# Kernel tuning notes

Measured on AMD Instinct MI355X. Metric: run time of the kernel, lower is better.

## Reference

```python
import jax, jax.numpy as jnp
import numpy as np

N = 384       # nodes
K = 60        # neighbors per node
SUB = 20      # subsample_k
C_S = 128
C_Z = 128
H = 4
D_HEAD = C_Z // H
NUM_RBF = 64
E = N * K
EPS = 1e-8


def _rbf(D, D_min=0.0, D_max=20.0, D_count=NUM_RBF):
    # radial basis expansion of distances: [..., ] -> [..., D_count]
    mu = jnp.linspace(D_min, D_max, D_count)
    sigma = (D_max - D_min) / D_count
    return jnp.exp(-(((D[..., None] - mu) / sigma) ** 2))


def setup_inputs() -> dict:
    key = jax.random.key(0)
    ks = jax.random.split(key, 16)
    f32 = jnp.float32
    inp = {
        "node_features": jax.random.normal(ks[0], (N, C_S), f32),
        "node_trans": jax.random.normal(ks[1], (N, 3), f32) * 5.0,
        "edge_features": jax.random.normal(ks[2], (E, C_Z), f32),
        "edge_index": jax.random.randint(ks[3], (2, E), 0, N),
        "subsample_idx": jax.random.randint(ks[4], (N, K, SUB), 0, K),
        # dist_bias_gate: Linear(2*c_s -> H)
        "W_gate": jax.random.normal(ks[5], (2 * C_S, H), f32) / np.sqrt(2 * C_S),
        "b_gate": jnp.zeros((H,), f32),
        # dist_bias: Linear(num_rbf -> H)
        "W_db": jax.random.normal(ks[6], (NUM_RBF, H), f32) / np.sqrt(NUM_RBF),
        "b_db": jnp.zeros((H,), f32),
        # lin_qk: Linear(c_z -> 2*c_z)
        "W_qk": jax.random.normal(ks[7], (C_Z, 2 * C_Z), f32) / np.sqrt(C_Z),
        "b_qk": jnp.zeros((2 * C_Z,), f32),
        # lin_v: Linear(c_z -> c_z)
        "W_v": jax.random.normal(ks[8], (C_Z, C_Z), f32) / np.sqrt(C_Z),
        "b_v": jnp.zeros((C_Z,), f32),
        # lin_out: Linear(c_z -> c_z) (init='final' in source; random here for testing)
        "W_out": jax.random.normal(ks[9], (C_Z, C_Z), f32) / np.sqrt(C_Z),
        "b_out": jnp.zeros((C_Z,), f32),
    }
    return inp


def reference(node_features, node_trans, edge_features, edge_index, subsample_idx,
              W_gate, b_gate, W_db, b_db, W_qk, b_qk, W_v, b_v, W_out, b_out):
    n, k, sub = subsample_idx.shape
    # assume_sorted=True path: edges are grouped k-per-destination-node
    dst = edge_index[0].reshape(n, k)                           # [n,k] neighbor ids
    edge1 = jnp.broadcast_to(dst[:, :, None], (n, k, sub))      # [n,k,sub]
    edge2 = jnp.take_along_axis(
        jnp.broadcast_to(dst[:, None, :], (n, k, k)), subsample_idx, axis=-1)  # [n,k,sub]

    f1 = node_features[edge1]                                   # [n,k,sub,c_s]
    f2 = node_features[edge2]
    gate = jax.nn.sigmoid(jnp.concatenate([f1, f2], axis=-1) @ W_gate + b_gate)  # [n,k,sub,H]

    t1 = node_trans[edge1]                                      # [n,k,sub,3]
    t2 = node_trans[edge2]
    dist = jnp.linalg.norm(t1 - t2 + EPS, axis=-1)              # [n,k,sub]
    bias = gate * (_rbf(dist) @ W_db + b_db)                    # [n,k,sub,H]

    edges = edge_features.reshape(n, k, C_Z)
    qk = edges @ W_qk + b_qk
    q, kk = jnp.split(qk, 2, axis=-1)
    q = q.reshape(n, k, H, D_HEAD)
    kk = kk.reshape(n, k, H, D_HEAD)

    batch = jnp.arange(n)[:, None, None]
    k_sub = kk[batch, subsample_idx]                            # [n,k,sub,H,d]
    attn = jnp.einsum('nkhd,nkshd->nksh', q, k_sub) / np.sqrt(C_Z) + bias
    attn = jax.nn.softmax(attn, axis=2)                         # softmax over subsample axis

    v = (edges @ W_v + b_v).reshape(n, k, H, D_HEAD)
    v_sub = v[batch, subsample_idx]                             # [n,k,sub,H,d]
    upd = jnp.einsum('nksh,nkshd->nkhd', attn, v_sub).reshape(n * k, C_Z)
    return upd @ W_out + b_out                                  # [E, c_z]
```

## Files before the change

### kernel.cpp

```cpp
#include <hip/hip_runtime.h>
#include <hip/hip_bf16.h>

typedef unsigned short ushortT;
typedef __attribute__((ext_vector_type(8))) short bf16x8;
typedef __attribute__((ext_vector_type(4))) float f32x4;
typedef __attribute__((ext_vector_type(2))) float f32x2;

#define N_NODES 384
#define KNBR 60
#define SUBK 20
#define NEDGE (N_NODES * KNBR)
#define EPSC 1e-8f
#define INV_SQRT_CZ 0.08838834764831845f
#define MU_STEP (20.0f / 63.0f)
#define INV_MU_STEP (63.0f / 20.0f)
#define INV_SIGMA 3.2f

__device__ __forceinline__ float bflo(unsigned int u) { return __uint_as_float(u << 16); }
__device__ __forceinline__ float bfhi(unsigned int u) { return __uint_as_float(u & 0xffff0000u); }
__device__ __forceinline__ f32x2 bfpair(unsigned int u) {
  f32x2 r;
  r.x = bflo(u);
  r.y = bfhi(u);
  return r;
}
__device__ __forceinline__ ushortT f2bu(float v) {
  union { float f; unsigned int u; } c;
  c.f = v;
  return (ushortT)((c.u + 0x7fffu + ((c.u >> 16) & 1u)) >> 16);
}
__device__ __forceinline__ unsigned int pack2bf(float x, float y) {
  return (unsigned int)f2bu(x) | ((unsigned int)f2bu(y) << 16);
}
__device__ __forceinline__ ushortT f2h(float x) {
  _Float16 h = (_Float16)x;
  return __builtin_bit_cast(ushortT, h);
}
__device__ __forceinline__ float h2f(ushortT u) {
  return (float)__builtin_bit_cast(_Float16, u);
}

__global__ __launch_bounds__(256) void prep_kernel(
    const float* __restrict__ nf, const float* __restrict__ Wg, float* __restrict__ g,
    const float* __restrict__ Wqk, const float* __restrict__ bqk,
    const float* __restrict__ Wv, const float* __restrict__ bv,
    const float* __restrict__ Wout,
    ushortT* __restrict__ Wp1, ushortT* __restrict__ Wp2, float* __restrict__ bc) {
  int b = blockIdx.x, tid = threadIdx.x;
  if (b < 96) {
    int n = b * 4 + (tid >> 6), t = tid & 63;
    float a = nf[n * 128 + t];
    float bb = nf[n * 128 + 64 + t];
    float acc[8];
#pragma unroll
    for (int h = 0; h < 4; ++h) {
      acc[h]     = a * Wg[t * 4 + h]         + bb * Wg[(t + 64) * 4 + h];
      acc[4 + h] = a * Wg[(128 + t) * 4 + h] + bb * Wg[(192 + t) * 4 + h];
    }
#pragma unroll
    for (int i = 0; i < 8; ++i)
#pragma unroll
      for (int off = 32; off >= 1; off >>= 1) acc[i] += __shfl_xor(acc[i], off, 64);
    if (t == 0) {
#pragma unroll
      for (int i = 0; i < 8; ++i) g[n * 8 + i] = acc[i];
    }
  } else {
    int i = (b - 96) * 256 + tid;
    if (i < 49152) {
      int j = i & 7, l = (i >> 3) & 63, t = (i >> 9) & 3;
      int nt = (i >> 11) % 12, ny = (i >> 11) / 12;
      int nn = ny * 192 + nt * 16 + (l & 15);
      int k = t * 32 + (l >> 4) * 8 + j;
      float v = (nn < 256) ? Wqk[k * 256 + nn] : Wv[k * 128 + (nn - 256)];
      if (nn < 128) v *= INV_SQRT_CZ;
      Wp1[i] = f2bu(v);
    } else {
      int i2 = i - 49152;
      int j = i2 & 7, l = (i2 >> 3) & 63, t = (i2 >> 9) & 3, nt = (i2 >> 11);
      int nn = nt * 16 + (l & 15);
      int k = t * 32 + (l >> 4) * 8 + j;
      Wp2[i2] = f2bu(Wout[k * 128 + nn]);
    }
    if (i < 384) {
      float v = (i < 256) ? bqk[i] : bv[i - 256];
      if (i < 128) v *= INV_SQRT_CZ;
      bc[i] = v;
    }
  }
}

__global__ __launch_bounds__(512, 4) void fused_kernel(
    const float* __restrict__ ef, const ushortT* __restrict__ Wp1,
    const ushortT* __restrict__ Wp2, const float* __restrict__ bc,
    const float* __restrict__ bout, const float* __restrict__ g,
    const float* __restrict__ node_trans, const int* __restrict__ edge_index,
    const int* __restrict__ sub_idx, const float* __restrict__ W_db,
    const float* __restrict__ b_db, const float* __restrict__ b_gate,
    float* __restrict__ outp) {
  __shared__ __align__(16) ushortT kvb[KNBR * 256];
  __shared__ __align__(16) ushortT updq[64 * 136];
  __shared__ __align__(16) ushortT biasb[KNBR * SUBK * 4];
  __shared__ ushortT sub_lds[KNBR * SUBK];

  int n = blockIdx.x, tid = threadIdx.x;
  int e0 = n * KNBR;
  int w = tid >> 6, l = tid & 63;
  int lr = l & 15, lc = l >> 4;
  int rowA = (w & 3) * 16 + lr;
  int rowAc = min(rowA, KNBR - 1);
  int Tbase = (tid >> 8) * 12;

  bf16x8 bcur[4], bnxt[4];
#pragma unroll
  for (int t = 0; t < 4; ++t)
    bcur[t] = *(const bf16x8*)(Wp1 + ((Tbase * 4 + t) * 64 + l) * 8);

  bf16x8 afrag[4];
#pragma unroll
  for (int t = 0; t < 4; ++t) {
    const float* ap = ef + (size_t)(e0 + rowAc) * 128 + t * 32 + lc * 8;
    float4 lo = *(const float4*)ap;
    float4 hi = *(const float4*)(ap + 4);
    bf16x8 a;
    a[0] = (short)f2bu(lo.x); a[1] = (short)f2bu(lo.y);
    a[2] = (short)f2bu(lo.z); a[3] = (short)f2bu(lo.w);
    a[4] = (short)f2bu(hi.x); a[5] = (short)f2bu(hi.y);
    a[6] = (short)f2bu(hi.z); a[7] = (short)f2bu(hi.w);
    afrag[t] = a;
  }

#pragma unroll
  for (int Ti = 0; Ti < 12; ++Ti) {
    int T = Tbase + Ti;
    if (Ti < 11) {
#pragma unroll
      for (int t = 0; t < 4; ++t)
        bnxt[t] = *(const bf16x8*)(Wp1 + (((T + 1) * 4 + t) * 64 + l) * 8);
    }
    f32x4 acc = {0.f, 0.f, 0.f, 0.f};
#pragma unroll
    for (int t = 0; t < 4; ++t)
      acc = __builtin_amdgcn_mfma_f32_16x16x32_bf16(bcur[t], afrag[t], acc, 0, 0, 0);
    int col0 = T * 16 + lc * 4;
    float4 bi = *(const float4*)(bc + col0);
    float o0 = acc[0] + bi.x, o1 = acc[1] + bi.y;
    float o2 = acc[2] + bi.z, o3 = acc[3] + bi.w;
    uint2 o;
    o.x = pack2bf(o0, o1);
    o.y = pack2bf(o2, o3);
    if (T < 8) {
      *(uint2*)(updq + rowA * 136 + col0) = o;
    } else if (rowA < KNBR) {
      int colk = col0 - 128;
      int base_b = (colk & 128) << 1;
      int d = colk & 127;
      int inner = ((d >> 3) & 1) * 128 + (((d >> 4) * 16) ^ ((rowA & 7) << 4)) + (d & 7) * 2;
      *(uint2*)((char*)kvb + rowA * 512 + base_b + inner) = o;
    }
#pragma unroll
    for (int t = 0; t < 4; ++t) bcur[t] = bnxt[t];
  }

  float4 bgv = *(const float4*)b_gate;
  float4 bdbv = *(const float4*)b_db;
  for (int p = tid; p < KNBR * SUBK; p += 512) {
    int kl = p / SUBK, s = p - kl * SUBK;
    int j = sub_idx[(size_t)(e0 + kl) * SUBK + s];
    sub_lds[p] = (ushortT)j;
    int dk = edge_index[e0 + kl];
    int dj = edge_index[e0 + j];
    float dx = node_trans[dk * 3 + 0] - node_trans[dj * 3 + 0] + EPSC;
    float dy = node_trans[dk * 3 + 1] - node_trans[dj * 3 + 1] + EPSC;
    float dz = node_trans[dk * 3 + 2] - node_trans[dj * 3 + 2] + EPSC;
    float dist = sqrtf(dx * dx + dy * dy + dz * dz);
    int r0 = (int)(dist * INV_MU_STEP + 0.5f);
    int rlo = max(r0 - 4, 0), rhi = min(r0 + 4, 63);
    float a0 = 0.f, a1 = 0.f, a2 = 0.f, a3 = 0.f;
    for (int r = rlo; r <= rhi; ++r) {
      float t = (dist - r * MU_STEP) * INV_SIGMA;
      float e = __expf(-t * t);
      float4 wv = ((const float4*)W_db)[r];
      a0 += e * wv.x; a1 += e * wv.y; a2 += e * wv.z; a3 += e * wv.w;
    }
    float4 gk = *(const float4*)(g + dk * 8);
    float4 gj = *(const float4*)(g + dj * 8 + 4);
    float g1 = gk.x + gj.x + bgv.x;
    float g2 = gk.y + gj.y + bgv.y;
    float g3 = gk.z + gj.z + bgv.z;
    float g4 = gk.w + gj.w + bgv.w;
    biasb[p * 4 + 0] = f2h((a0 + bdbv.x) / (1.0f + __expf(-g1)));
    biasb[p * 4 + 1] = f2h((a1 + bdbv.y) / (1.0f + __expf(-g2)));
    biasb[p * 4 + 2] = f2h((a2 + bdbv.z) / (1.0f + __expf(-g3)));
    biasb[p * 4 + 3] = f2h((a3 + bdbv.w) / (1.0f + __expf(-g4)));
  }
  __syncthreads();

  int row3 = tid >> 3, h = (tid >> 1) & 3, dh = tid & 1;
  int row3c = min(row3, KNBR - 1);
  int hdo = (h * 2 + dh) * 16;
  const char* kvbase = (const char*)kvb;
  f32x2 qv0, qv1, qv2, qv3, qv4, qv5, qv6, qv7;
  {
    const ushortT* qp = updq + row3 * 136 + h * 32 + dh * 16;
    uint4 u0 = *(const uint4*)qp;
    uint4 u1 = *(const uint4*)(qp + 8);
    qv0 = bfpair(u0.x); qv1 = bfpair(u0.y); qv2 = bfpair(u0.z); qv3 = bfpair(u0.w);
    qv4 = bfpair(u1.x); qv5 = bfpair(u1.y); qv6 = bfpair(u1.z); qv7 = bfpair(u1.w);
  }
  float den = 0.f;
  f32x2 va0 = {0.f, 0.f}, va1 = {0.f, 0.f}, va2 = {0.f, 0.f}, va3 = {0.f, 0.f};
  f32x2 va4 = {0.f, 0.f}, va5 = {0.f, 0.f}, va6 = {0.f, 0.f}, va7 = {0.f, 0.f};
#pragma unroll 4
  for (int s = 0; s < SUBK; ++s) {
    int j = sub_lds[row3c * SUBK + s];
    int off = hdo ^ ((j & 7) << 4);
    const char* kr = kvbase + j * 512;
    uint4 k0 = *(const uint4*)(kr + off);
    uint4 k1 = *(const uint4*)(kr + 128 + off);
    f32x2 dacc = qv0 * bfpair(k0.x);
    dacc += qv1 * bfpair(k0.y);
    dacc += qv2 * bfpair(k0.z);
    dacc += qv3 * bfpair(k0.w);
    dacc += qv4 * bfpair(k1.x);
    dacc += qv5 * bfpair(k1.y);
    dacc += qv6 * bfpair(k1.z);
    dacc += qv7 * bfpair(k1.w);
    float dot = dacc.x + dacc.y;
    dot += __shfl_xor(dot, 1);
    float p = __expf(dot + h2f(biasb[(row3c * SUBK + s) * 4 + h]));
    den += p;
    f32x2 pp = {p, p};
    uint4 w0 = *(const uint4*)(kr + 256 + off);
    uint4 w1 = *(const uint4*)(kr + 384 + off);
    va0 += pp * bfpair(w0.x);
    va1 += pp * bfpair(w0.y);
    va2 += pp * bfpair(w0.z);
    va3 += pp * bfpair(w0.w);
    va4 += pp * bfpair(w1.x);
    va5 += pp * bfpair(w1.y);
    va6 += pp * bfpair(w1.z);
    va7 += pp * bfpair(w1.w);
  }
  float inv = 1.0f / den;
  {
    uint4 o;
    o.x = pack2bf(va0.x * inv, va0.y * inv);
    o.y = pack2bf(va1.x * inv, va1.y * inv);
    o.z = pack2bf(va2.x * inv, va2.y * inv);
    o.w = pack2bf(va3.x * inv, va3.y * inv);
    *(uint4*)(updq + row3 * 136 + h * 32 + dh * 16) = o;
    uint4 o2;
    o2.x = pack2bf(va4.x * inv, va4.y * inv);
    o2.y = pack2bf(va5.x * inv, va5.y * inv);
    o2.z = pack2bf(va6.x * inv, va6.y * inv);
    o2.w = pack2bf(va7.x * inv, va7.y * inv);
    *(uint4*)(updq + row3 * 136 + h * 32 + dh * 16 + 8) = o2;
  }
  __syncthreads();

  int T4base = (tid >> 8) * 4;
  bf16x8 af2[4];
#pragma unroll
  for (int t = 0; t < 4; ++t)
    af2[t] = *(const bf16x8*)(updq + rowA * 136 + t * 32 + lc * 8);
  bf16x8 c2[4], n2[4];
#pragma unroll
  for (int t = 0; t < 4; ++t)
    c2[t] = *(const bf16x8*)(Wp2 + ((T4base * 4 + t) * 64 + l) * 8);
#pragma unroll
  for (int Ti = 0; Ti < 4; ++Ti) {
    int T = T4base + Ti;
    if (Ti < 3) {
#pragma unroll
      for (int t = 0; t < 4; ++t)
        n2[t] = *(const bf16x8*)(Wp2 + (((T + 1) * 4 + t) * 64 + l) * 8);
    }
    f32x4 acc = {0.f, 0.f, 0.f, 0.f};
#pragma unroll
    for (int t = 0; t < 4; ++t)
      acc = __builtin_amdgcn_mfma_f32_16x16x32_bf16(c2[t], af2[t], acc, 0, 0, 0);
    if (rowA < KNBR) {
      int col0 = T * 16 + lc * 4;
      float4 bi = *(const float4*)(bout + col0);
      float4 o;
      o.x = acc[0] + bi.x; o.y = acc[1] + bi.y;
      o.z = acc[2] + bi.z; o.w = acc[3] + bi.w;
      *(float4*)(outp + (size_t)(e0 + rowA) * 128 + col0) = o;
    }
#pragma unroll
    for (int t = 0; t < 4; ++t) c2[t] = n2[t];
  }
}

extern "C" void kernel_launch(void* const* d_in, const int* in_sizes, int n_in, void* d_out,
                              int out_size, void* d_ws, size_t ws_size, hipStream_t stream) {
  const float* nf  = (const float*)d_in[0];
  const float* nt  = (const float*)d_in[1];
  const float* ef  = (const float*)d_in[2];
  const int*   ei  = (const int*)d_in[3];
  const int*   si  = (const int*)d_in[4];
  const float* Wg  = (const float*)d_in[5];
  const float* bg  = (const float*)d_in[6];
  const float* Wdb = (const float*)d_in[7];
  const float* bdb = (const float*)d_in[8];
  const float* Wqk = (const float*)d_in[9];
  const float* bqk = (const float*)d_in[10];
  const float* Wv  = (const float*)d_in[11];
  const float* bv  = (const float*)d_in[12];
  const float* Wout = (const float*)d_in[13];
  const float* bout = (const float*)d_in[14];
  float* out = (float*)d_out;

  float* g      = (float*)d_ws;
  float* bc     = g + 3072;
  ushortT* Wp1  = (ushortT*)(bc + 384);
  ushortT* Wp2  = Wp1 + 49152;

  prep_kernel<<<dim3(352), dim3(256), 0, stream>>>(nf, Wg, g, Wqk, bqk, Wv, bv, Wout,
                                                   Wp1, Wp2, bc);
  fused_kernel<<<dim3(N_NODES), dim3(512), 0, stream>>>(ef, Wp1, Wp2, bc, bout, g, nt, ei, si,
                                                        Wdb, bdb, bg, out);
}
```

Before: 40.53 us.

## Split fused per-node kernel into projection/bias and attention/output kernels

The single per-node fused kernel (384 blocks, 4 of 12 rows idle in MFMA tiles) is split into a projection+bias kernel spread over 1260 blocks and an attention+output-projection kernel with 720 blocks of 32 edges each. Q, K/V and bias are now round-tripped through global workspace in bf16/fp16 instead of living in LDS. This is meant to raise parallelism and occupancy on a GPU with many CUs, removing padding waste. In exchange it adds extra global memory traffic, an extra launch, and uncoalesced gathers of K/V rows from global memory.

```diff
diff --git a/kernel.cpp b/kernel.cpp
--- a/kernel.cpp
+++ b/kernel.cpp
@@ -15,14 +15,13 @@
 #define MU_STEP (20.0f / 63.0f)
 #define INV_MU_STEP (63.0f / 20.0f)
 #define INV_SIGMA 3.2f
+#define QKV_BLOCKS 360
+#define BIAS_BLOCKS 900
 
 __device__ __forceinline__ float bflo(unsigned int u) { return __uint_as_float(u << 16); }
 __device__ __forceinline__ float bfhi(unsigned int u) { return __uint_as_float(u & 0xffff0000u); }
 __device__ __forceinline__ f32x2 bfpair(unsigned int u) {
-  f32x2 r;
-  r.x = bflo(u);
-  r.y = bfhi(u);
-  return r;
+  f32x2 r; r.x = bflo(u); r.y = bfhi(u); return r;
 }
 __device__ __forceinline__ ushortT f2bu(float v) {
   union { float f; unsigned int u; } c;
@@ -90,134 +89,121 @@
   }
 }
 
-__global__ __launch_bounds__(512, 4) void fused_kernel(
+__global__ __launch_bounds__(512) void proj_bias_kernel(
     const float* __restrict__ ef, const ushortT* __restrict__ Wp1,
-    const ushortT* __restrict__ Wp2, const float* __restrict__ bc,
-    const float* __restrict__ bout, const float* __restrict__ g,
-    const float* __restrict__ node_trans, const int* __restrict__ edge_index,
-    const int* __restrict__ sub_idx, const float* __restrict__ W_db,
+    const float* __restrict__ bc, const int* __restrict__ ei,
+    const int* __restrict__ si, const float* __restrict__ nt,
+    const float* __restrict__ g, const float* __restrict__ W_db,
     const float* __restrict__ b_db, const float* __restrict__ b_gate,
-    float* __restrict__ outp) {
-  __shared__ __align__(16) ushortT kvb[KNBR * 256];
-  __shared__ __align__(16) ushortT updq[64 * 136];
-  __shared__ __align__(16) ushortT biasb[KNBR * SUBK * 4];
-  __shared__ ushortT sub_lds[KNBR * SUBK];
-
-  int n = blockIdx.x, tid = threadIdx.x;
-  int e0 = n * KNBR;
-  int w = tid >> 6, l = tid & 63;
-  int lr = l & 15, lc = l >> 4;
-  int rowA = (w & 3) * 16 + lr;
-  int rowAc = min(rowA, KNBR - 1);
-  int Tbase = (tid >> 8) * 12;
-
-  bf16x8 bcur[4], bnxt[4];
-#pragma unroll
-  for (int t = 0; t < 4; ++t)
-    bcur[t] = *(const bf16x8*)(Wp1 + ((Tbase * 4 + t) * 64 + l) * 8);
-
-  bf16x8 afrag[4];
-#pragma unroll
-  for (int t = 0; t < 4; ++t) {
-    const float* ap = ef + (size_t)(e0 + rowAc) * 128 + t * 32 + lc * 8;
-    float4 lo = *(const float4*)ap;
-    float4 hi = *(const float4*)(ap + 4);
-    bf16x8 a;
-    a[0] = (short)f2bu(lo.x); a[1] = (short)f2bu(lo.y);
-    a[2] = (short)f2bu(lo.z); a[3] = (short)f2bu(lo.w);
-    a[4] = (short)f2bu(hi.x); a[5] = (short)f2bu(hi.y);
-    a[6] = (short)f2bu(hi.z); a[7] = (short)f2bu(hi.w);
-    afrag[t] = a;
-  }
-
-#pragma unroll
-  for (int Ti = 0; Ti < 12; ++Ti) {
-    int T = Tbase + Ti;
-    if (Ti < 11) {
-#pragma unroll
-      for (int t = 0; t < 4; ++t)
-        bnxt[t] = *(const bf16x8*)(Wp1 + (((T + 1) * 4 + t) * 64 + l) * 8);
-    }
-    f32x4 acc = {0.f, 0.f, 0.f, 0.f};
-#pragma unroll
-    for (int t = 0; t < 4; ++t)
-      acc = __builtin_amdgcn_mfma_f32_16x16x32_bf16(bcur[t], afrag[t], acc, 0, 0, 0);
-    int col0 = T * 16 + lc * 4;
-    float4 bi = *(const float4*)(bc + col0);
-    float o0 = acc[0] + bi.x, o1 = acc[1] + bi.y;
-    float o2 = acc[2] + bi.z, o3 = acc[3] + bi.w;
-    uint2 o;
-    o.x = pack2bf(o0, o1);
-    o.y = pack2bf(o2, o3);
-    if (T < 8) {
-      *(uint2*)(updq + rowA * 136 + col0) = o;
-    } else if (rowA < KNBR) {
-      int colk = col0 - 128;
-      int base_b = (colk & 128) << 1;
-      int d = colk & 127;
-      int inner = ((d >> 3) & 1) * 128 + (((d >> 4) * 16) ^ ((rowA & 7) << 4)) + (d & 7) * 2;
-      *(uint2*)((char*)kvb + rowA * 512 + base_b + inner) = o;
-    }
-#pragma unroll
-    for (int t = 0; t < 4; ++t) bcur[t] = bnxt[t];
-  }
-
-  float4 bgv = *(const float4*)b_gate;
-  float4 bdbv = *(const float4*)b_db;
-  for (int p = tid; p < KNBR * SUBK; p += 512) {
-    int kl = p / SUBK, s = p - kl * SUBK;
-    int j = sub_idx[(size_t)(e0 + kl) * SUBK + s];
-    sub_lds[p] = (ushortT)j;
-    int dk = edge_index[e0 + kl];
-    int dj = edge_index[e0 + j];
-    float dx = node_trans[dk * 3 + 0] - node_trans[dj * 3 + 0] + EPSC;
-    float dy = node_trans[dk * 3 + 1] - node_trans[dj * 3 + 1] + EPSC;
-    float dz = node_trans[dk * 3 + 2] - node_trans[dj * 3 + 2] + EPSC;
+    ushortT* __restrict__ qws, ushortT* __restrict__ kvws,
+    ushortT* __restrict__ biasws) {
+  int b = blockIdx.x, tid = threadIdx.x;
+  if (b < QKV_BLOCKS) {
+    int w = tid >> 6, l = tid & 63;
+    int lr = l & 15, lc = l >> 4;
+    int row = b * 64 + (w & 3) * 16 + lr;
+    int Tbase = (tid >> 8) * 12;
+    bf16x8 afrag[4];
+#pragma unroll
+    for (int t = 0; t < 4; ++t) {
+      const float* ap = ef + (size_t)row * 128 + t * 32 + lc * 8;
+      float4 lo = *(const float4*)ap;
+      float4 hi = *(const float4*)(ap + 4);
+      bf16x8 a;
+      a[0] = (short)f2bu(lo.x); a[1] = (short)f2bu(lo.y);
+      a[2] = (short)f2bu(lo.z); a[3] = (short)f2bu(lo.w);
+      a[4] = (short)f2bu(hi.x); a[5] = (short)f2bu(hi.y);
+      a[6] = (short)f2bu(hi.z); a[7] = (short)f2bu(hi.w);
+      afrag[t] = a;
+    }
+#pragma unroll
+    for (int Ti = 0; Ti < 12; ++Ti) {
+      int T = Tbase + Ti;
+      f32x4 acc = {0.f, 0.f, 0.f, 0.f};
+#pragma unroll
+      for (int t = 0; t < 4; ++t) {
+        bf16x8 bfrag = *(const bf16x8*)(Wp1 + ((T * 4 + t) * 64 + l) * 8);
+        acc = __builtin_amdgcn_mfma_f32_16x16x32_bf16(bfrag, afrag[t], acc, 0, 0, 0);
+      }
+      int col0 = T * 16 + lc * 4;
+      float4 bi = *(const float4*)(bc + col0);
+      uint2 o;
+      o.x = pack2bf(acc[0] + bi.x, acc[1] + bi.y);
+      o.y = pack2bf(acc[2] + bi.z, acc[3] + bi.w);
+      if (T < 8) {
+        *(uint2*)(qws + (size_t)row * 128 + col0) = o;
+      } else {
+        *(uint2*)(kvws + (size_t)row * 256 + (col0 - 128)) = o;
+      }
+    }
+  } else {
+    int p = (b - QKV_BLOCKS) * 512 + tid;
+    int e = p / SUBK, s = p - e * SUBK;
+    int n = e / KNBR;
+    int j = si[p];
+    int dk = ei[e];
+    int dj = ei[n * KNBR + j];
+    float dx = nt[dk * 3 + 0] - nt[dj * 3 + 0] + EPSC;
+    float dy = nt[dk * 3 + 1] - nt[dj * 3 + 1] + EPSC;
+    float dz = nt[dk * 3 + 2] - nt[dj * 3 + 2] + EPSC;
     float dist = sqrtf(dx * dx + dy * dy + dz * dz);
     int r0 = (int)(dist * INV_MU_STEP + 0.5f);
     int rlo = max(r0 - 4, 0), rhi = min(r0 + 4, 63);
     float a0 = 0.f, a1 = 0.f, a2 = 0.f, a3 = 0.f;
     for (int r = rlo; r <= rhi; ++r) {
       float t = (dist - r * MU_STEP) * INV_SIGMA;
-      float e = __expf(-t * t);
+      float eexp = __expf(-t * t);
       float4 wv = ((const float4*)W_db)[r];
-      a0 += e * wv.x; a1 += e * wv.y; a2 += e * wv.z; a3 += e * wv.w;
-    }
+      a0 += eexp * wv.x; a1 += eexp * wv.y; a2 += eexp * wv.z; a3 += eexp * wv.w;
+    }
+    float4 bgv = *(const float4*)b_gate;
+    float4 bdbv = *(const float4*)b_db;
     float4 gk = *(const float4*)(g + dk * 8);
     float4 gj = *(const float4*)(g + dj * 8 + 4);
     float g1 = gk.x + gj.x + bgv.x;
     float g2 = gk.y + gj.y + bgv.y;
     float g3 = gk.z + gj.z + bgv.z;
     float g4 = gk.w + gj.w + bgv.w;
-    biasb[p * 4 + 0] = f2h((a0 + bdbv.x) / (1.0f + __expf(-g1)));
-    biasb[p * 4 + 1] = f2h((a1 + bdbv.y) / (1.0f + __expf(-g2)));
-    biasb[p * 4 + 2] = f2h((a2 + bdbv.z) / (1.0f + __expf(-g3)));
-    biasb[p * 4 + 3] = f2h((a3 + bdbv.w) / (1.0f + __expf(-g4)));
-  }
-  __syncthreads();
-
-  int row3 = tid >> 3, h = (tid >> 1) & 3, dh = tid & 1;
-  int row3c = min(row3, KNBR - 1);
-  int hdo = (h * 2 + dh) * 16;
-  const char* kvbase = (const char*)kvb;
+    uint2 o;
+    o.x = (unsigned int)f2h((a0 + bdbv.x) / (1.0f + __expf(-g1))) |
+          ((unsigned int)f2h((a1 + bdbv.y) / (1.0f + __expf(-g2))) << 16);
+    o.y = (unsigned int)f2h((a2 + bdbv.z) / (1.0f + __expf(-g3))) |
+          ((unsigned int)f2h((a3 + bdbv.w) / (1.0f + __expf(-g4))) << 16);
+    *(uint2*)(biasws + (size_t)p * 4) = o;
+  }
+}
+
+__global__ __launch_bounds__(256) void attn_out_kernel(
+    const ushortT* __restrict__ qws, const ushortT* __restrict__ kvws,
+    const ushortT* __restrict__ biasws, const int* __restrict__ si,
+    const ushortT* __restrict__ Wp2, const float* __restrict__ bout,
+    float* __restrict__ outp) {
+  __shared__ __align__(16) ushortT updb[32 * 136];
+  int b = blockIdx.x, tid = threadIdx.x;
+  int le = tid >> 3, h = (tid >> 1) & 3, dh = tid & 1;
+  int e = b * 32 + le;
+  int n = e / KNBR;
+  int jbase = n * KNBR;
+
   f32x2 qv0, qv1, qv2, qv3, qv4, qv5, qv6, qv7;
   {
-    const ushortT* qp = updq + row3 * 136 + h * 32 + dh * 16;
+    const ushortT* qp = qws + (size_t)e * 128 + h * 32 + dh * 16;
     uint4 u0 = *(const uint4*)qp;
     uint4 u1 = *(const uint4*)(qp + 8);
     qv0 = bfpair(u0.x); qv1 = bfpair(u0.y); qv2 = bfpair(u0.z); qv3 = bfpair(u0.w);
     qv4 = bfpair(u1.x); qv5 = bfpair(u1.y); qv6 = bfpair(u1.z); qv7 = bfpair(u1.w);
   }
+  const int* sip = si + (size_t)e * SUBK;
+  const ushortT* bp = biasws + (size_t)e * (SUBK * 4);
   float den = 0.f;
   f32x2 va0 = {0.f, 0.f}, va1 = {0.f, 0.f}, va2 = {0.f, 0.f}, va3 = {0.f, 0.f};
   f32x2 va4 = {0.f, 0.f}, va5 = {0.f, 0.f}, va6 = {0.f, 0.f}, va7 = {0.f, 0.f};
-#pragma unroll 4
+#pragma unroll
   for (int s = 0; s < SUBK; ++s) {
-    int j = sub_lds[row3c * SUBK + s];
-    int off = hdo ^ ((j & 7) << 4);
-    const char* kr = kvbase + j * 512;
-    uint4 k0 = *(const uint4*)(kr + off);
-    uint4 k1 = *(const uint4*)(kr + 128 + off);
+    int j = sip[s];
+    const ushortT* kr = kvws + (size_t)(jbase + j) * 256 + h * 32 + dh * 16;
+    uint4 k0 = *(const uint4*)kr;
+    uint4 k1 = *(const uint4*)(kr + 8);
     f32x2 dacc = qv0 * bfpair(k0.x);
     dacc += qv1 * bfpair(k0.y);
     dacc += qv2 * bfpair(k0.z);
@@ -228,11 +214,12 @@
     dacc += qv7 * bfpair(k1.w);
     float dot = dacc.x + dacc.y;
     dot += __shfl_xor(dot, 1);
-    float p = __expf(dot + h2f(biasb[(row3c * SUBK + s) * 4 + h]));
+    float p = __expf(dot + h2f(bp[s * 4 + h]));
     den += p;
+    const ushortT* vr = kr + 128;
+    uint4 w0 = *(const uint4*)vr;
+    uint4 w1 = *(const uint4*)(vr + 8);
     f32x2 pp = {p, p};
-    uint4 w0 = *(const uint4*)(kr + 256 + off);
-    uint4 w1 = *(const uint4*)(kr + 384 + off);
     va0 += pp * bfpair(w0.x);
     va1 += pp * bfpair(w0.y);
     va2 += pp * bfpair(w0.z);
@@ -249,47 +236,37 @@
     o.y = pack2bf(va1.x * inv, va1.y * inv);
     o.z = pack2bf(va2.x * inv, va2.y * inv);
     o.w = pack2bf(va3.x * inv, va3.y * inv);
-    *(uint4*)(updq + row3 * 136 + h * 32 + dh * 16) = o;
+    *(uint4*)(updb + le * 136 + h * 32 + dh * 16) = o;
     uint4 o2;
     o2.x = pack2bf(va4.x * inv, va4.y * inv);
     o2.y = pack2bf(va5.x * inv, va5.y * inv);
     o2.z = pack2bf(va6.x * inv, va6.y * inv);
     o2.w = pack2bf(va7.x * inv, va7.y * inv);
-    *(uint4*)(updq + row3 * 136 + h * 32 + dh * 16 + 8) = o2;
+    *(uint4*)(updb + le * 136 + h * 32 + dh * 16 + 8) = o2;
   }
   __syncthreads();
 
-  int T4base = (tid >> 8) * 4;
+  int w = tid >> 6, l = tid & 63, lr = l & 15, lc = l >> 4;
+  int lrow = (w & 1) * 16 + lr;
   bf16x8 af2[4];
 #pragma unroll
   for (int t = 0; t < 4; ++t)
-    af2[t] = *(const bf16x8*)(updq + rowA * 136 + t * 32 + lc * 8);
-  bf16x8 c2[4], n2[4];
-#pragma unroll
-  for (int t = 0; t < 4; ++t)
-    c2[t] = *(const bf16x8*)(Wp2 + ((T4base * 4 + t) * 64 + l) * 8);
+    af2[t] = *(const bf16x8*)(updb + lrow * 136 + t * 32 + lc * 8);
 #pragma unroll
   for (int Ti = 0; Ti < 4; ++Ti) {
-    int T = T4base + Ti;
-    if (Ti < 3) {
-#pragma unroll
-      for (int t = 0; t < 4; ++t)
-        n2[t] = *(const bf16x8*)(Wp2 + (((T + 1) * 4 + t) * 64 + l) * 8);
-    }
+    int T = (w >> 1) * 4 + Ti;
     f32x4 acc = {0.f, 0.f, 0.f, 0.f};
 #pragma unroll
-    for (int t = 0; t < 4; ++t)
-      acc = __builtin_amdgcn_mfma_f32_16x16x32_bf16(c2[t], af2[t], acc, 0, 0, 0);
-    if (rowA < KNBR) {
-      int col0 = T * 16 + lc * 4;
-      float4 bi = *(const float4*)(bout + col0);
-      float4 o;
-      o.x = acc[0] + bi.x; o.y = acc[1] + bi.y;
-      o.z = acc[2] + bi.z; o.w = acc[3] + bi.w;
-      *(float4*)(outp + (size_t)(e0 + rowA) * 128 + col0) = o;
-    }
-#pragma unroll
-    for (int t = 0; t < 4; ++t) c2[t] = n2[t];
+    for (int t = 0; t < 4; ++t) {
+      bf16x8 bfrag = *(const bf16x8*)(Wp2 + ((T * 4 + t) * 64 + l) * 8);
+      acc = __builtin_amdgcn_mfma_f32_16x16x32_bf16(bfrag, af2[t], acc, 0, 0, 0);
+    }
+    int col0 = T * 16 + lc * 4;
+    float4 bi = *(const float4*)(bout + col0);
+    float4 o;
+    o.x = acc[0] + bi.x; o.y = acc[1] + bi.y;
+    o.z = acc[2] + bi.z; o.w = acc[3] + bi.w;
+    *(float4*)(outp + (size_t)(b * 32 + lrow) * 128 + col0) = o;
   }
 }
 
@@ -312,13 +289,18 @@
   const float* bout = (const float*)d_in[14];
   float* out = (float*)d_out;
 
-  float* g      = (float*)d_ws;
-  float* bc     = g + 3072;
-  ushortT* Wp1  = (ushortT*)(bc + 384);
-  ushortT* Wp2  = Wp1 + 49152;
+  float* g       = (float*)d_ws;
+  float* bc      = g + 3072;
+  ushortT* Wp1   = (ushortT*)(bc + 384);
+  ushortT* Wp2   = Wp1 + 49152;
+  ushortT* qws   = Wp2 + 16384;
+  ushortT* kvws  = qws + (size_t)NEDGE * 128;
+  ushortT* biasws = kvws + (size_t)NEDGE * 256;
 
   prep_kernel<<<dim3(352), dim3(256), 0, stream>>>(nf, Wg, g, Wqk, bqk, Wv, bv, Wout,
                                                    Wp1, Wp2, bc);
-  fused_kernel<<<dim3(N_NODES), dim3(512), 0, stream>>>(ef, Wp1, Wp2, bc, bout, g, nt, ei, si,
-                                                        Wdb, bdb, bg, out);
-}
+  proj_bias_kernel<<<dim3(QKV_BLOCKS + BIAS_BLOCKS), dim3(512), 0, stream>>>(
+      ef, Wp1, bc, ei, si, nt, g, Wdb, bdb, bg, qws, kvws, biasws);
+  attn_out_kernel<<<dim3(NEDGE / 32), dim3(256), 0, stream>>>(qws, kvws, biasws, si, Wp2,
+                                                              bout, out);
+}
```

Result: slower. 57.97 us (+43.0%).
